# Optimization experiments

Measured on AMD Instinct MI355X. Metric: run time of the kernel, lower is better.

The kernel has to match this reference:

```python
import jax, jax.numpy as jnp
import numpy as np

CHAN = 128
IN_CHAN = 3
NB_OUT = 10
K = 2  # maxPoolKer


def affine_grid(theta, H, W):
    # theta: [C,2,3] -> grid [C,H,W,2], torch F.affine_grid align_corners=False
    xs = (2.0 * jnp.arange(W, dtype=jnp.float32) + 1.0) / W - 1.0
    ys = (2.0 * jnp.arange(H, dtype=jnp.float32) + 1.0) / H - 1.0
    gx, gy = jnp.meshgrid(xs, ys)  # [H,W]
    base = jnp.stack([gx, gy, jnp.ones_like(gx)], axis=-1)  # [H,W,3]
    return jnp.einsum('crk,hwk->chwr', theta, base)  # [...,0]=x, [...,1]=y


def grid_sample(img, grid):
    # img [M,H,W], grid [M,H,W,2]; bilinear, zeros padding, align_corners=False
    M, H, W = img.shape
    ix = ((grid[..., 0] + 1.0) * W - 1.0) * 0.5
    iy = ((grid[..., 1] + 1.0) * H - 1.0) * 0.5
    x0 = jnp.floor(ix)
    y0 = jnp.floor(iy)
    wx = ix - x0
    wy = iy - y0

    def tap(xi, yi):
        valid = (xi >= 0) & (xi <= W - 1) & (yi >= 0) & (yi <= H - 1)
        xc = jnp.clip(xi, 0, W - 1).astype(jnp.int32)
        yc = jnp.clip(yi, 0, H - 1).astype(jnp.int32)
        v = jax.vmap(lambda im, y, x: im[y, x])(img, yc, xc)
        return jnp.where(valid, v, 0.0)

    v00 = tap(x0, y0)
    v01 = tap(x0 + 1.0, y0)
    v10 = tap(x0, y0 + 1.0)
    v11 = tap(x0 + 1.0, y0 + 1.0)
    return (1.0 - wy) * ((1.0 - wx) * v00 + wx * v01) + wy * ((1.0 - wx) * v10 + wx * v11)


def geom_layer(x, geo, lin, box):
    # x [B,Ci,H,W]; lin [C,Ci]; geo,box [C,2,3]
    B, Ci, H, W = x.shape
    C = lin.shape[0]
    y = jnp.einsum('ci,bihw->bchw', lin, x)  # channel linear combine
    grid = affine_grid(geo, H, W)            # [C,H,W,2], shared across batch
    samp = jax.vmap(lambda yb: grid_sample(yb, grid))(y)  # [B,C,H,W]
    bgrid = affine_grid(box, H, W)
    boxm = grid_sample(jnp.ones((C, H, W), samp.dtype), bgrid)  # BoxPool mask
    return samp * boxm[None]


def maxpool_g(x, k):
    # MaxPool2d_G: depthwise box-filter conv -> argmax -> gather window from padded x
    B, C, H, W = x.shape
    ch, cw = H // k, W // k
    ker = jnp.ones((1, 1, ch, cw), x.dtype) / (ch + cw)
    xr = x.reshape(B * C, 1, H, W)
    conv = jax.lax.conv_general_dilated(
        xr, ker, (1, 1), [(ch // 2, ch // 2), (cw // 2, cw // 2)])
    conv = conv[:, :, :H, :W].reshape(B, C, H * W)
    argm = jnp.argmax(conv, axis=-1)
    r = argm // H  # original code uses origImgSize[0]; assumes square H==W
    c = argm % W
    padH, padW = H + H // k, W + W // k
    top = padH // 2 - H // 2
    left = padW // 2 - W // 2
    padded = jnp.zeros((B, C, padH, padW), x.dtype).at[:, :, top:top + H, left:left + W].set(x)
    r2 = r + H // (2 * k)
    c2 = c + W // (2 * k)
    ri = r2[..., None] + (jnp.arange(ch) - ch // 2)  # [B,C,ch]
    ci = c2[..., None] + (jnp.arange(cw) - cw // 2)  # [B,C,cw]
    gat = jax.vmap(jax.vmap(lambda p, rr, cc: p[rr[:, None], cc[None, :]]))(padded, ri, ci)
    return gat  # [B,C,ch,cw]


def setup_inputs() -> dict:
    key = jax.random.key(0)
    ks = jax.random.split(key, 12)
    eye = jnp.eye(3, dtype=jnp.float32)[:2]  # [2,3]
    x = jax.random.normal(ks[0], (8, IN_CHAN, 64, 64), dtype=jnp.float32)
    geo0 = eye[None] + 0.1 * jax.random.normal(ks[1], (CHAN, 2, 3), dtype=jnp.float32)
    lin0 = jax.random.uniform(ks[2], (CHAN, IN_CHAN), dtype=jnp.float32)
    box0 = eye[None] + 0.1 * jax.random.normal(ks[3], (CHAN, 2, 3), dtype=jnp.float32)
    geos = eye[None, None] + 0.1 * jax.random.normal(ks[4], (3, CHAN, 2, 3), dtype=jnp.float32)
    lins = jax.random.uniform(ks[5], (3, CHAN, CHAN), dtype=jnp.float32)
    boxes = eye[None, None] + 0.1 * jax.random.normal(ks[6], (3, CHAN, 2, 3), dtype=jnp.float32)
    bound = 1.0 / np.sqrt(CHAN)
    dense_w = jax.random.uniform(ks[7], (NB_OUT, CHAN), dtype=jnp.float32, minval=-bound, maxval=bound)
    dense_b = jax.random.uniform(ks[8], (NB_OUT,), dtype=jnp.float32, minval=-bound, maxval=bound)
    return {"x": x, "geo0": geo0, "lin0": lin0, "box0": box0,
            "geos": geos, "lins": lins, "boxes": boxes,
            "dense_w": dense_w, "dense_b": dense_b}


def reference(x, geo0, lin0, box0, geos, lins, boxes, dense_w, dense_b):
    h = geom_layer(x, geo0, lin0, box0)            # inLay: [8,128,64,64]
    h = geom_layer(h, geos[0], lins[0], boxes[0])  # layer 0
    h = maxpool_g(h, K)                            # layer 1 (maxPoolPos=1): [8,128,32,32]
    h = geom_layer(h, geos[1], lins[1], boxes[1])  # layer 2
    h = geom_layer(h, geos[2], lins[2], boxes[2])  # layer 3
    feat = h
    pooled = feat.mean(axis=-1).mean(axis=-1)      # [B,C]
    out = pooled @ dense_w.T + dense_b             # [B,nbOut]
    return out, feat
```

## Files before the change

### kernel.cpp

```cpp
#include <hip/hip_runtime.h>

#define BB 8
#define CC 128

typedef _Float16 f16x4 __attribute__((ext_vector_type(4)));
typedef float f32x4 __attribute__((ext_vector_type(4)));
typedef __fp16 fp16x2 __attribute__((ext_vector_type(2)));

__device__ __forceinline__ unsigned int pack2(float a, float b) {
  union { fp16x2 h; unsigned int u; } cv;
  cv.h = __builtin_amdgcn_cvt_pkrtz(a, b);
  return cv.u;
}

__device__ __forceinline__ float sample_pad(const float* __restrict__ pl, int stride,
                                            float WF, float ix, float iy) {
  ix = fminf(fmaxf(ix, -1.0f), WF);
  iy = fminf(fmaxf(iy, -1.0f), WF);
  float x0f = floorf(ix), y0f = floorf(iy);
  float wx = ix - x0f, wy = iy - y0f;
  int xi = (int)x0f + 1, yi = (int)y0f + 1;
  const float* p0 = pl + yi * stride + xi;
  float v00 = p0[0], v01 = p0[1], v10 = p0[stride], v11 = p0[stride + 1];
  return (1.0f - wy) * ((1.0f - wx) * v00 + wx * v01) +
         wy * ((1.0f - wx) * v10 + wx * v11);
}

__device__ __forceinline__ float box_mask(float bix, float biy, float WM1) {
  float bx0 = floorf(bix), by0 = floorf(biy);
  float bwx = bix - bx0, bwy = biy - by0;
  float mx = (((bx0 >= 0.0f) && (bx0 <= WM1)) ? (1.0f - bwx) : 0.0f) +
             (((bx0 >= -1.0f) && (bx0 <= WM1 - 1.0f)) ? bwx : 0.0f);
  float my = (((by0 >= 0.0f) && (by0 <= WM1)) ? (1.0f - bwy) : 0.0f) +
             (((by0 >= -1.0f) && (by0 <= WM1 - 1.0f)) ? bwy : 0.0f);
  return mx * my;
}

__global__ __launch_bounds__(256) void inlay_sample_kernel(
    const float* __restrict__ x, const float* __restrict__ lin,
    const float* __restrict__ geo, const float* __restrict__ box,
    const float* __restrict__ db, float* __restrict__ out,
    float* __restrict__ head) {
  const int H = 64, W = 64, HW = 4096;
  __shared__ float cp[67 * 68];
  int bc = blockIdx.x;
  int c = bc & (CC - 1);
  int b = bc >> 7;
  int tid = threadIdx.x;
  if (bc == 0 && tid < 80) head[tid] = db[tid % 10];
  const float* xb = x + (size_t)b * 3 * HW;

  float w0 = lin[c * 3 + 0], w1 = lin[c * 3 + 1], w2 = lin[c * 3 + 2];

  if (tid < 68) {
    cp[tid] = 0.0f; cp[65 * 68 + tid] = 0.0f; cp[66 * 68 + tid] = 0.0f;
  } else if (tid < 132) {
    int r = tid - 67;
    cp[r * 68 + 0] = 0.0f; cp[r * 68 + 65] = 0.0f; cp[r * 68 + 66] = 0.0f;
  }

#pragma unroll
  for (int k = 0; k < 4; ++k) {
    int i4 = tid + k * 256;
    int base = i4 * 4;
    float4 f0 = *reinterpret_cast<const float4*>(&xb[base]);
    float4 f1 = *reinterpret_cast<const float4*>(&xb[HW + base]);
    float4 f2 = *reinterpret_cast<const float4*>(&xb[2 * HW + base]);
    int h = i4 >> 4, w = (i4 & 15) * 4;
    float* d = &cp[(h + 1) * 68 + w + 1];
    d[0] = w0 * f0.x + w1 * f1.x + w2 * f2.x;
    d[1] = w0 * f0.y + w1 * f1.y + w2 * f2.y;
    d[2] = w0 * f0.z + w1 * f1.z + w2 * f2.z;
    d[3] = w0 * f0.w + w1 * f1.w + w2 * f2.w;
  }
  __syncthreads();

  const float* g = geo + c * 6;
  const float* bx = box + c * 6;
  float a0 = 32.0f * g[0], a1 = 32.0f * g[1], a2 = 32.0f * g[2] + 31.5f;
  float a3 = 32.0f * g[3], a4 = 32.0f * g[4], a5 = 32.0f * g[5] + 31.5f;
  float c0 = 32.0f * bx[0], c1 = 32.0f * bx[1], c2 = 32.0f * bx[2] + 31.5f;
  float c3 = 32.0f * bx[3], c4 = 32.0f * bx[4], c5 = 32.0f * bx[5] + 31.5f;
  float* o = out + ((size_t)b * CC + c) * HW;

#pragma unroll
  for (int k = 0; k < 16; ++k) {
    int px = tid + k * 256;
    int h = px >> 6, w = px & 63;
    float xs = (2.0f * w + 1.0f) / W - 1.0f;
    float ys = (2.0f * h + 1.0f) / H - 1.0f;
    float ix = fmaf(a0, xs, fmaf(a1, ys, a2));
    float iy = fmaf(a3, xs, fmaf(a4, ys, a5));
    float samp = sample_pad(cp, 68, 64.0f, ix, iy);
    float bix = fmaf(c0, xs, fmaf(c1, ys, c2));
    float biy = fmaf(c3, xs, fmaf(c4, ys, c5));
    o[px] = samp * box_mask(bix, biy, 63.0f);
  }
}

__global__ __launch_bounds__(256) void gemm64_mfma_kernel(
    const float* __restrict__ lin, const float* __restrict__ x,
    float* __restrict__ y) {
  const int Ci = 128, HW = 4096;
  __shared__ unsigned int A_lds[64 * 66];
  __shared__ unsigned int B_lds[64 * 66];
  int b = blockIdx.z;
  int row0 = blockIdx.y * 64, col0 = blockIdx.x * 64;
  const float* xb = x + (size_t)b * Ci * HW;
  float* yb = y + (size_t)b * CC * HW;
  int tid = threadIdx.x;

  {
    int row = tid >> 2, kc = (tid & 3) * 32;
    const float* ap = &lin[(row0 + row) * Ci + kc];
    unsigned int* dst = &A_lds[row * 66 + (kc >> 1)];
#pragma unroll
    for (int i = 0; i < 8; ++i) {
      float4 v = *reinterpret_cast<const float4*>(ap + i * 4);
      dst[i * 2] = pack2(v.x, v.y);
      dst[i * 2 + 1] = pack2(v.z, v.w);
    }
  }
  {
    int kp = tid >> 2, cg = (tid & 3) * 16;
    const float* b0p = &xb[(size_t)(2 * kp) * HW + col0 + cg];
    const float* b1p = &xb[(size_t)(2 * kp + 1) * HW + col0 + cg];
#pragma unroll
    for (int q = 0; q < 4; ++q) {
      float4 v0 = *reinterpret_cast<const float4*>(b0p + q * 4);
      float4 v1 = *reinterpret_cast<const float4*>(b1p + q * 4);
      unsigned int* bp_ = &B_lds[(cg + q * 4) * 66 + kp];
      bp_[0 * 66] = pack2(v0.x, v1.x);
      bp_[1 * 66] = pack2(v0.y, v1.y);
      bp_[2 * 66] = pack2(v0.z, v1.z);
      bp_[3 * 66] = pack2(v0.w, v1.w);
    }
  }
  __syncthreads();

  int w = tid >> 6, l = tid & 63;
  int lr = l & 15, lq = l >> 4;
  f32x4 acc0 = {0.f, 0.f, 0.f, 0.f};
  f32x4 acc1 = acc0, acc2 = acc0, acc3 = acc0;
  const unsigned int* arow = &A_lds[(w * 16 + lr) * 66 + 2 * lq];
  const unsigned int* bcol = &B_lds[lr * 66 + 2 * lq];
#pragma unroll
  for (int s = 0; s < 8; ++s) {
    f16x4 af = *reinterpret_cast<const f16x4*>(arow + s * 8);
    f16x4 b0 = *reinterpret_cast<const f16x4*>(bcol + 0 * 16 * 66 + s * 8);
    f16x4 b1 = *reinterpret_cast<const f16x4*>(bcol + 1 * 16 * 66 + s * 8);
    f16x4 b2 = *reinterpret_cast<const f16x4*>(bcol + 2 * 16 * 66 + s * 8);
    f16x4 b3 = *reinterpret_cast<const f16x4*>(bcol + 3 * 16 * 66 + s * 8);
    acc0 = __builtin_amdgcn_mfma_f32_16x16x16f16(af, b0, acc0, 0, 0, 0);
    acc1 = __builtin_amdgcn_mfma_f32_16x16x16f16(af, b1, acc1, 0, 0, 0);
    acc2 = __builtin_amdgcn_mfma_f32_16x16x16f16(af, b2, acc2, 0, 0, 0);
    acc3 = __builtin_amdgcn_mfma_f32_16x16x16f16(af, b3, acc3, 0, 0, 0);
  }
#pragma unroll
  for (int i = 0; i < 4; ++i) {
    float* yr = yb + (size_t)(row0 + w * 16 + lq * 4 + i) * HW + col0 + lr;
    yr[0]  = acc0[i];
    yr[16] = acc1[i];
    yr[32] = acc2[i];
    yr[48] = acc3[i];
  }
}

__global__ __launch_bounds__(256) void gemm32_mfma_kernel(
    const float* __restrict__ lin, const float* __restrict__ x,
    float* __restrict__ y) {
  const int Ci = 128, HW = 1024;
  __shared__ unsigned int A_lds[32 * 66];
  __shared__ unsigned int B_lds[64 * 66];
  int b = blockIdx.z;
  int row0 = blockIdx.y * 32, col0 = blockIdx.x * 64;
  const float* xb = x + (size_t)b * Ci * HW;
  float* yb = y + (size_t)b * CC * HW;
  int tid = threadIdx.x;

  {
    int row = tid >> 3, kc = (tid & 7) * 16;
    const float* ap = &lin[(row0 + row) * Ci + kc];
    unsigned int* dst = &A_lds[row * 66 + (kc >> 1)];
#pragma unroll
    for (int i = 0; i < 4; ++i) {
      float4 v = *reinterpret_cast<const float4*>(ap + i * 4);
      dst[i * 2] = pack2(v.x, v.y);
      dst[i * 2 + 1] = pack2(v.z, v.w);
    }
  }
  {
    int kp = tid >> 2, cg = (tid & 3) * 16;
    const float* b0p = &xb[(size_t)(2 * kp) * HW + col0 + cg];
    const float* b1p = &xb[(size_t)(2 * kp + 1) * HW + col0 + cg];
#pragma unroll
    for (int q = 0; q < 4; ++q) {
      float4 v0 = *reinterpret_cast<const float4*>(b0p + q * 4);
      float4 v1 = *reinterpret_cast<const float4*>(b1p + q * 4);
      unsigned int* bp_ = &B_lds[(cg + q * 4) * 66 + kp];
      bp_[0 * 66] = pack2(v0.x, v1.x);
      bp_[1 * 66] = pack2(v0.y, v1.y);
      bp_[2 * 66] = pack2(v0.z, v1.z);
      bp_[3 * 66] = pack2(v0.w, v1.w);
    }
  }
  __syncthreads();

  int w = tid >> 6, l = tid & 63;
  int lr = l & 15, lq = l >> 4;
  int rs = (w & 1) * 16;
  int ct0 = (w >> 1) * 2;
  f32x4 acc0 = {0.f, 0.f, 0.f, 0.f};
  f32x4 acc1 = acc0;
  const unsigned int* arow = &A_lds[(rs + lr) * 66 + 2 * lq];
  const unsigned int* bc0 = &B_lds[(ct0 * 16 + lr) * 66 + 2 * lq];
  const unsigned int* bc1 = &B_lds[((ct0 + 1) * 16 + lr) * 66 + 2 * lq];
#pragma unroll
  for (int s = 0; s < 8; ++s) {
    f16x4 af = *reinterpret_cast<const f16x4*>(arow + s * 8);
    f16x4 b0 = *reinterpret_cast<const f16x4*>(bc0 + s * 8);
    f16x4 b1 = *reinterpret_cast<const f16x4*>(bc1 + s * 8);
    acc0 = __builtin_amdgcn_mfma_f32_16x16x16f16(af, b0, acc0, 0, 0, 0);
    acc1 = __builtin_amdgcn_mfma_f32_16x16x16f16(af, b1, acc1, 0, 0, 0);
  }
#pragma unroll
  for (int i = 0; i < 4; ++i) {
    float* yr = yb + (size_t)(row0 + rs + lq * 4 + i) * HW + col0 + ct0 * 16 + lr;
    yr[0]  = acc0[i];
    yr[16] = acc1[i];
  }
}

__global__ __launch_bounds__(256) void sampmax_kernel(
    const float* __restrict__ y, const float* __restrict__ geo,
    const float* __restrict__ box, float* __restrict__ out) {
  __shared__ __align__(16) float sp[64 * 68];
  __shared__ __align__(16) float arena[67 * 68];
  __shared__ float wv[4];
  __shared__ int wi[4];
  __shared__ int am_s;
  float* pl = arena;
  float* cb = arena;

  int bc = blockIdx.x;
  int c = bc & (CC - 1);
  int tid = threadIdx.x;

  if (tid < 68) {
    pl[tid] = 0.0f; pl[65 * 68 + tid] = 0.0f; pl[66 * 68 + tid] = 0.0f;
  } else if (tid < 132) {
    int r = tid - 67;
    pl[r * 68 + 0] = 0.0f; pl[r * 68 + 65] = 0.0f; pl[r * 68 + 66] = 0.0f;
  }
  {
    const float* plane = y + (size_t)bc * 4096;
#pragma unroll
    for (int k = 0; k < 4; ++k) {
      int i4 = tid + k * 256;
      float4 f = *reinterpret_cast<const float4*>(&plane[i4 * 4]);
      int h = i4 >> 4, w = (i4 & 15) * 4;
      float* d = &pl[(h + 1) * 68 + w + 1];
      d[0] = f.x; d[1] = f.y; d[2] = f.z; d[3] = f.w;
    }
  }
  __syncthreads();

  {
    const float* g = geo + c * 6;
    const float* bx = box + c * 6;
    float a0 = 32.0f * g[0], a1 = 32.0f * g[1], a2 = 32.0f * g[2] + 31.5f;
    float a3 = 32.0f * g[3], a4 = 32.0f * g[4], a5 = 32.0f * g[5] + 31.5f;
    float c0 = 32.0f * bx[0], c1 = 32.0f * bx[1], c2 = 32.0f * bx[2] + 31.5f;
    float c3 = 32.0f * bx[3], c4 = 32.0f * bx[4], c5 = 32.0f * bx[5] + 31.5f;
#pragma unroll
    for (int k = 0; k < 16; ++k) {
      int px = tid + k * 256;
      int h = px >> 6, w = px & 63;
      float xs = (2.0f * w + 1.0f) / 64.0f - 1.0f;
      float ys = (2.0f * h + 1.0f) / 64.0f - 1.0f;
      float ix = fmaf(a0, xs, fmaf(a1, ys, a2));
      float iy = fmaf(a3, xs, fmaf(a4, ys, a5));
      float samp = sample_pad(pl, 68, 64.0f, ix, iy);
      float bix = fmaf(c0, xs, fmaf(c1, ys, c2));
      float biy = fmaf(c3, xs, fmaf(c4, ys, c5));
      sp[h * 68 + w] = samp * box_mask(bix, biy, 63.0f);
    }
  }
  __syncthreads();

  {
    int strip = tid >> 4, w4 = (tid & 15) * 4;
    int h0 = strip * 4;
    float4 a = make_float4(0.f, 0.f, 0.f, 0.f);
    float4 keep0 = a, keep1 = a, keep2 = a;
#pragma unroll
    for (int j = 0; j < 32; ++j) {
      int r = h0 + j - 16;
      bool valid = (r >= 0) && (r < 64);
      int rc = valid ? r : 0;
      float4 f = *reinterpret_cast<const float4*>(&sp[rc * 68 + w4]);
      f.x = valid ? f.x : 0.0f; f.y = valid ? f.y : 0.0f;
      f.z = valid ? f.z : 0.0f; f.w = valid ? f.w : 0.0f;
      if (j == 0) keep0 = f;
      if (j == 1) keep1 = f;
      if (j == 2) keep2 = f;
      a.x += f.x; a.y += f.y; a.z += f.z; a.w += f.w;
    }
    *reinterpret_cast<float4*>(&cb[(h0 + 0) * 68 + w4]) = a;
#pragma unroll
    for (int j = 32; j < 35; ++j) {
      int r = h0 + j - 16;
      bool valid = (r < 64);
      int rc = valid ? r : 0;
      float4 f = *reinterpret_cast<const float4*>(&sp[rc * 68 + w4]);
      f.x = valid ? f.x : 0.0f; f.y = valid ? f.y : 0.0f;
      f.z = valid ? f.z : 0.0f; f.w = valid ? f.w : 0.0f;
      float4 kp = (j == 32) ? keep0 : ((j == 33) ? keep1 : keep2);
      a.x += f.x - kp.x; a.y += f.y - kp.y; a.z += f.z - kp.z; a.w += f.w - kp.w;
      *reinterpret_cast<float4*>(&cb[(h0 + j - 31) * 68 + w4]) = a;
    }
  }
  __syncthreads();

  float best = -3.402823466e+38f;
  int bidx = 0x7fffffff;
#pragma unroll
  for (int hh = 0; hh < 4; ++hh) {
    int h = (tid >> 4) + hh * 16;
    int w4 = (tid & 15) * 4;
    float s0 = 0.f, k0 = 0.f, k1 = 0.f, k2 = 0.f;
#pragma unroll
    for (int q = 0; q < 8; ++q) {
      int u0 = w4 - 16 + 4 * q;
      bool ok = (u0 >= 0) && (u0 <= 60);
      int uc = ok ? u0 : 0;
      float4 f = *reinterpret_cast<const float4*>(&cb[h * 68 + uc]);
      f.x = ok ? f.x : 0.0f; f.y = ok ? f.y : 0.0f;
      f.z = ok ? f.z : 0.0f; f.w = ok ? f.w : 0.0f;
      if (q == 0) { k0 = f.x; k1 = f.y; k2 = f.z; }
      s0 += f.x; s0 += f.y; s0 += f.z; s0 += f.w;
    }
    float ftx = 0.f, fty = 0.f, ftz = 0.f;
    {
      int u0 = w4 + 16;
      bool ok = (u0 <= 60);
      int uc = ok ? u0 : 0;
      float4 f = *reinterpret_cast<const float4*>(&cb[h * 68 + uc]);
      ftx = ok ? f.x : 0.0f; fty = ok ? f.y : 0.0f; ftz = ok ? f.z : 0.0f;
    }
    float s1 = s0 - k0 + ftx;
    float s2 = s1 - k1 + fty;
    float s3 = s2 - k2 + ftz;
    float sv[4] = {s0, s1, s2, s3};
#pragma unroll
    for (int d = 0; d < 4; ++d) {
      int i = (h << 6) + w4 + d;
      if (sv[d] > best) { best = sv[d]; bidx = i; }
    }
  }
#pragma unroll
  for (int off = 32; off > 0; off >>= 1) {
    float v2 = __shfl_down(best, off);
    int i2 = __shfl_down(bidx, off);
    if (v2 > best || (v2 == best && i2 < bidx)) { best = v2; bidx = i2; }
  }
  if ((tid & 63) == 0) { wv[tid >> 6] = best; wi[tid >> 6] = bidx; }
  __syncthreads();
  if (tid == 0) {
    float bv = wv[0]; int bi = wi[0];
#pragma unroll
    for (int k = 1; k < 4; ++k)
      if (wv[k] > bv || (wv[k] == bv && wi[k] < bi)) { bv = wv[k]; bi = wi[k]; }
    am_s = bi;
  }
  __syncthreads();

  int am = am_s;
  int r = am >> 6, cx = am & 63;
  float* o = out + (size_t)bc * 1024;
#pragma unroll
  for (int k = 0; k < 4; ++k) {
    int idx = tid + k * 256;
    int oi = idx >> 5, oj = idx & 31;
    int rr = r + oi - 16, cj = cx + oj - 16;
    bool v = (rr >= 0) && (rr < 64) && (cj >= 0) && (cj < 64);
    int rrc = v ? rr : 0, cjc = v ? cj : 0;
    o[idx] = v ? sp[rrc * 68 + cjc] : 0.0f;
  }
}

template <bool POOL>
__global__ __launch_bounds__(256) void sample32_kernel(
    const float* __restrict__ y, const float* __restrict__ geo,
    const float* __restrict__ box, float* __restrict__ out,
    const float* __restrict__ dw, float* __restrict__ head) {
  const int W = 32, HW = 1024;
  __shared__ float pl[35 * 36];
  __shared__ float wred[4];
  int bc = blockIdx.x;
  int c = bc & (CC - 1);
  int b = bc >> 7;
  int tid = threadIdx.x;

  if (tid < 36) {
    pl[tid] = 0.0f; pl[33 * 36 + tid] = 0.0f; pl[34 * 36 + tid] = 0.0f;
  } else if (tid < 68) {
    int r = tid - 35;
    pl[r * 36 + 0] = 0.0f; pl[r * 36 + 33] = 0.0f; pl[r * 36 + 34] = 0.0f; pl[r * 36 + 35] = 0.0f;
  }
  {
    const float* plane = y + (size_t)bc * HW;
    float4 f = *reinterpret_cast<const float4*>(&plane[tid * 4]);
    int h = tid >> 3, w = (tid & 7) * 4;
    float* d = &pl[(h + 1) * 36 + w + 1];
    d[0] = f.x; d[1] = f.y; d[2] = f.z; d[3] = f.w;
  }
  __syncthreads();

  const float* g = geo + c * 6;
  const float* bxp = box + c * 6;
  float a0 = 16.0f * g[0], a1 = 16.0f * g[1], a2 = 16.0f * g[2] + 15.5f;
  float a3 = 16.0f * g[3], a4 = 16.0f * g[4], a5 = 16.0f * g[5] + 15.5f;
  float c0 = 16.0f * bxp[0], c1 = 16.0f * bxp[1], c2 = 16.0f * bxp[2] + 15.5f;
  float c3 = 16.0f * bxp[3], c4 = 16.0f * bxp[4], c5 = 16.0f * bxp[5] + 15.5f;
  float* o = out + (size_t)bc * HW;
  float psum = 0.f;
#pragma unroll
  for (int k = 0; k < 4; ++k) {
    int px = tid + k * 256;
    int h = px >> 5, w = px & 31;
    float xs = (2.0f * w + 1.0f) / W - 1.0f;
    float ys = (2.0f * h + 1.0f) / W - 1.0f;
    float ix = fmaf(a0, xs, fmaf(a1, ys, a2));
    float iy = fmaf(a3, xs, fmaf(a4, ys, a5));
    float samp = sample_pad(pl, 36, 32.0f, ix, iy);
    float bix = fmaf(c0, xs, fmaf(c1, ys, c2));
    float biy = fmaf(c3, xs, fmaf(c4, ys, c5));
    float res = samp * box_mask(bix, biy, 31.0f);
    o[px] = res;
    if (POOL) psum += res;
  }
  if (POOL) {
    int lane = tid & 63, wid = tid >> 6;
    float r = psum;
#pragma unroll
    for (int off = 32; off > 0; off >>= 1) r += __shfl_down(r, off);
    if (lane == 0) wred[wid] = r;
    __syncthreads();
    if (tid < 10) {
      float t = (wred[0] + wred[1] + wred[2] + wred[3]) * (1.0f / 1024.0f);
      atomicAdd(&head[b * 10 + tid], t * dw[tid * 128 + c]);
    }
  }
}

extern "C" void kernel_launch(void* const* d_in, const int* in_sizes, int n_in,
                              void* d_out, int out_size, void* d_ws, size_t ws_size,
                              hipStream_t stream) {
  const float* x     = (const float*)d_in[0];
  const float* geo0  = (const float*)d_in[1];
  const float* lin0  = (const float*)d_in[2];
  const float* box0  = (const float*)d_in[3];
  const float* geos  = (const float*)d_in[4];
  const float* lins  = (const float*)d_in[5];
  const float* boxes = (const float*)d_in[6];
  const float* dw    = (const float*)d_in[7];
  const float* db    = (const float*)d_in[8];

  float* out  = (float*)d_out;
  float* feat = out + 80;
  float* ws   = (float*)d_ws;
  float* ws0  = ws;
  float* ws1  = ws + 4194304;
  float* ws2  = ws + 8388608;

  inlay_sample_kernel<<<dim3(BB * CC), 256, 0, stream>>>(x, lin0, geo0, box0, db, ws1, out);
  gemm64_mfma_kernel<<<dim3(64, 2, BB), 256, 0, stream>>>(lins, ws1, ws0);
  sampmax_kernel<<<dim3(BB * CC), 256, 0, stream>>>(ws0, geos, boxes, ws1);
  gemm32_mfma_kernel<<<dim3(16, 4, BB), 256, 0, stream>>>(lins + 16384, ws1, ws2);
  sample32_kernel<false><<<dim3(BB * CC), 256, 0, stream>>>(ws2, geos + 768, boxes + 768, ws0, nullptr, nullptr);
  gemm32_mfma_kernel<<<dim3(16, 4, BB), 256, 0, stream>>>(lins + 32768, ws0, ws2);
  sample32_kernel<true><<<dim3(BB * CC), 256, 0, stream>>>(ws2, geos + 1536, boxes + 1536, feat, dw, out);
}
```

Measured before the change: 137.8 us.

## Restructure box-filter argmax into per-lane sliding windows with transposed LDS buffer

Rewrites the separable 32x32 box-filter in sampmax_kernel so each wave covers a 16-row (then 16-column) band and each lane slides a running sum down one column. A register ring buffer holds the values leaving the window, and the intermediate column sums go to a transposed LDS buffer with stride 65 to avoid bank conflicts. This replaces the float4 strip scheme with its 8-wide horizontal re-summation, reducing redundant LDS reads and adds. It also adds a min-blocks-per-CU hint of 4 to launch bounds; the 32-entry register rings could raise register pressure under that cap.

```diff
diff --git a/kernel.cpp b/kernel.cpp
--- a/kernel.cpp
+++ b/kernel.cpp
@@ -231,7 +231,7 @@
   }
 }
 
-__global__ __launch_bounds__(256) void sampmax_kernel(
+__global__ __launch_bounds__(256, 4) void sampmax_kernel(
     const float* __restrict__ y, const float* __restrict__ geo,
     const float* __restrict__ box, float* __restrict__ out) {
   __shared__ __align__(16) float sp[64 * 68];
@@ -240,7 +240,7 @@
   __shared__ int wi[4];
   __shared__ int am_s;
   float* pl = arena;
-  float* cb = arena;
+  float* cb2 = arena;
 
   int bc = blockIdx.x;
   int c = bc & (CC - 1);
@@ -289,73 +289,62 @@
   __syncthreads();
 
   {
-    int strip = tid >> 4, w4 = (tid & 15) * 4;
-    int h0 = strip * 4;
-    float4 a = make_float4(0.f, 0.f, 0.f, 0.f);
-    float4 keep0 = a, keep1 = a, keep2 = a;
+    int wv_ = tid >> 6;
+    int u = tid & 63;
+    int R0 = wv_ * 16;
+    float ring[32];
+    float S = 0.f;
 #pragma unroll
     for (int j = 0; j < 32; ++j) {
-      int r = h0 + j - 16;
+      int r = R0 - 16 + j;
       bool valid = (r >= 0) && (r < 64);
       int rc = valid ? r : 0;
-      float4 f = *reinterpret_cast<const float4*>(&sp[rc * 68 + w4]);
-      f.x = valid ? f.x : 0.0f; f.y = valid ? f.y : 0.0f;
-      f.z = valid ? f.z : 0.0f; f.w = valid ? f.w : 0.0f;
-      if (j == 0) keep0 = f;
-      if (j == 1) keep1 = f;
-      if (j == 2) keep2 = f;
-      a.x += f.x; a.y += f.y; a.z += f.z; a.w += f.w;
-    }
-    *reinterpret_cast<float4*>(&cb[(h0 + 0) * 68 + w4]) = a;
-#pragma unroll
-    for (int j = 32; j < 35; ++j) {
-      int r = h0 + j - 16;
-      bool valid = (r < 64);
-      int rc = valid ? r : 0;
-      float4 f = *reinterpret_cast<const float4*>(&sp[rc * 68 + w4]);
-      f.x = valid ? f.x : 0.0f; f.y = valid ? f.y : 0.0f;
-      f.z = valid ? f.z : 0.0f; f.w = valid ? f.w : 0.0f;
-      float4 kp = (j == 32) ? keep0 : ((j == 33) ? keep1 : keep2);
-      a.x += f.x - kp.x; a.y += f.y - kp.y; a.z += f.z - kp.z; a.w += f.w - kp.w;
-      *reinterpret_cast<float4*>(&cb[(h0 + j - 31) * 68 + w4]) = a;
+      float v = sp[rc * 68 + u];
+      v = valid ? v : 0.0f;
+      ring[j] = v;
+      S += v;
+    }
+#pragma unroll
+    for (int t = 0; t < 16; ++t) {
+      cb2[u * 65 + R0 + t] = S;
+      int rin = R0 + 16 + t;
+      bool vin = rin < 64;
+      int rc = vin ? rin : 0;
+      float fin = sp[rc * 68 + u];
+      fin = vin ? fin : 0.0f;
+      S += fin - ring[t];
     }
   }
   __syncthreads();
 
   float best = -3.402823466e+38f;
   int bidx = 0x7fffffff;
-#pragma unroll
-  for (int hh = 0; hh < 4; ++hh) {
-    int h = (tid >> 4) + hh * 16;
-    int w4 = (tid & 15) * 4;
-    float s0 = 0.f, k0 = 0.f, k1 = 0.f, k2 = 0.f;
-#pragma unroll
-    for (int q = 0; q < 8; ++q) {
-      int u0 = w4 - 16 + 4 * q;
-      bool ok = (u0 >= 0) && (u0 <= 60);
-      int uc = ok ? u0 : 0;
-      float4 f = *reinterpret_cast<const float4*>(&cb[h * 68 + uc]);
-      f.x = ok ? f.x : 0.0f; f.y = ok ? f.y : 0.0f;
-      f.z = ok ? f.z : 0.0f; f.w = ok ? f.w : 0.0f;
-      if (q == 0) { k0 = f.x; k1 = f.y; k2 = f.z; }
-      s0 += f.x; s0 += f.y; s0 += f.z; s0 += f.w;
-    }
-    float ftx = 0.f, fty = 0.f, ftz = 0.f;
-    {
-      int u0 = w4 + 16;
-      bool ok = (u0 <= 60);
-      int uc = ok ? u0 : 0;
-      float4 f = *reinterpret_cast<const float4*>(&cb[h * 68 + uc]);
-      ftx = ok ? f.x : 0.0f; fty = ok ? f.y : 0.0f; ftz = ok ? f.z : 0.0f;
-    }
-    float s1 = s0 - k0 + ftx;
-    float s2 = s1 - k1 + fty;
-    float s3 = s2 - k2 + ftz;
-    float sv[4] = {s0, s1, s2, s3};
-#pragma unroll
-    for (int d = 0; d < 4; ++d) {
-      int i = (h << 6) + w4 + d;
-      if (sv[d] > best) { best = sv[d]; bidx = i; }
+  {
+    int wv_ = tid >> 6;
+    int lane_r = tid & 63;
+    int C0 = wv_ * 16;
+    float ring2[32];
+    float S2 = 0.f;
+#pragma unroll
+    for (int j = 0; j < 32; ++j) {
+      int uu = C0 - 16 + j;
+      bool valid = (uu >= 0) && (uu < 64);
+      int uc = valid ? uu : 0;
+      float v = cb2[uc * 65 + lane_r];
+      v = valid ? v : 0.0f;
+      ring2[j] = v;
+      S2 += v;
+    }
+#pragma unroll
+    for (int t = 0; t < 16; ++t) {
+      int i = (lane_r << 6) + C0 + t;
+      if (S2 > best) { best = S2; bidx = i; }
+      int uin = C0 + 16 + t;
+      bool vin = uin < 64;
+      int uc = vin ? uin : 0;
+      float fin = cb2[uc * 65 + lane_r];
+      fin = vin ? fin : 0.0f;
+      S2 += fin - ring2[t];
     }
   }
 #pragma unroll
```

Result: no change. 136.7 us (median of 2 runs) (-0.9%).
